# Performance work log

Measured on AMD Instinct MI355X. Metric: run time of the kernel, lower is better.

The kernel has to match this reference:

```python
import jax, jax.numpy as jnp
import numpy as np
import math

N_HEAD = 16
ROPE_BASE = 10000.0


def _rope_cos_sin(seq_len, head_dim, dtype):
    # standard RoPE tables: freqs_i = base^(-2i/d), i in [0, d/2)
    half = head_dim // 2
    inv_freq = ROPE_BASE ** (-(jnp.arange(half, dtype=jnp.float32) * 2.0 / head_dim))
    t = jnp.arange(seq_len, dtype=jnp.float32)
    ang = t[:, None] * inv_freq[None, :]  # [S, d/2]
    return jnp.cos(ang).astype(dtype), jnp.sin(ang).astype(dtype)


def _apply_rope(x, cos, sin):
    # x: [B, S, H, d]; rotate interleaved even/odd pairs
    x1 = x[..., 0::2]
    x2 = x[..., 1::2]
    c = cos[None, :, None, :]
    s = sin[None, :, None, :]
    out = jnp.stack([x1 * c - x2 * s, x1 * s + x2 * c], axis=-1)
    return out.reshape(x.shape)


def setup_inputs() -> dict:
    key = jax.random.key(0)
    kx, kq, kk, kv, ko = jax.random.split(key, 5)
    B, S, H = 2, 2048, 1024
    x = jax.random.normal(kx, (B, S, H), dtype=jnp.float32)
    scale = 0.02
    w_q = jax.random.normal(kq, (H, H), dtype=jnp.float32) * scale
    w_k = jax.random.normal(kk, (H, H), dtype=jnp.float32) * scale
    w_v = jax.random.normal(kv, (H, H), dtype=jnp.float32) * scale
    w_o = jax.random.normal(ko, (H, H), dtype=jnp.float32) * scale
    return {"x": x, "w_q": w_q, "w_k": w_k, "w_v": w_v, "w_o": w_o}


def reference(x, w_q, w_k, w_v, w_o):
    B, S, H = x.shape
    d = H // N_HEAD
    # torch nn.Linear(bias=False): y = x @ W^T, W is [out, in]
    q = (x @ w_q.T).reshape(B, S, N_HEAD, d)
    k = (x @ w_k.T).reshape(B, S, N_HEAD, d)
    v = (x @ w_v.T).reshape(B, S, N_HEAD, d)
    cos, sin = _rope_cos_sin(S, d, x.dtype)
    q = _apply_rope(q, cos, sin)
    k = _apply_rope(k, cos, sin)
    scores = jnp.einsum("bqhd,bkhd->bhqk", q, k) / math.sqrt(d)
    coefs = jax.nn.softmax(scores, axis=-1)
    # NOTE: causal mask is applied AFTER softmax via tril (no renormalization)
    causal = jnp.tril(jnp.ones((S, S), dtype=bool))
    coefs = jnp.where(causal[None, None], coefs, 0.0)
    out = jnp.einsum("bhqk,bkhd->bqhd", coefs, v).reshape(B, S, H)
    return out @ w_o.T
```

## Files before the change

### kernel.cpp

```cpp
#include <hip/hip_runtime.h>
#include <math.h>

#define SEQ   2048
#define HDIM  1024
#define NH    16
#define DH    64
#define MTOT  4096
#define BHTOT 32

typedef _Float16 half_t;
typedef __attribute__((ext_vector_type(2))) __fp16 fp16x2;
typedef __attribute__((ext_vector_type(4))) _Float16 half4;
typedef __attribute__((ext_vector_type(8))) _Float16 half8;
typedef __attribute__((ext_vector_type(4))) float float4v;

typedef __attribute__((address_space(1))) const unsigned int guint;
typedef __attribute__((address_space(3))) unsigned int luint;
__device__ __forceinline__ void glds16(const half_t* g, half_t* l) {
    __builtin_amdgcn_global_load_lds((guint*)g, (luint*)l, 16, 0, 0);
}

__global__ __launch_bounds__(256)
void prep(const float* __restrict__ x,  const float* __restrict__ wq,
          const float* __restrict__ wk, const float* __restrict__ wv,
          const float* __restrict__ wo,
          half_t* __restrict__ xh,  half_t* __restrict__ wqh,
          half_t* __restrict__ wkh, half_t* __restrict__ wvh,
          half_t* __restrict__ woh, float2* __restrict__ rope)
{
    const int bid = blockIdx.x;
    if (bid < 8192) {
        int i = bid * 256 + threadIdx.x;
        const float* s; half_t* d;
        if (i < 1048576) { s = x; d = xh; }
        else {
            int j = i - 1048576;
            int w = j >> 18; i = j & 262143;
            s = (w == 0) ? wq : (w == 1) ? wk : (w == 2) ? wv : wo;
            d = (w == 0) ? wqh : (w == 1) ? wkh : (w == 2) ? wvh : woh;
        }
        float4 v = ((const float4*)s)[i];
        union { half_t h[4]; uint2 u; } tmp;
        tmp.h[0] = (half_t)v.x; tmp.h[1] = (half_t)v.y;
        tmp.h[2] = (half_t)v.z; tmp.h[3] = (half_t)v.w;
        ((uint2*)d)[i] = tmp.u;
    } else {
        int tt = (bid - 8192) * 256 + threadIdx.x;
        int s = tt >> 5, j = tt & 31;
        float inv = powf(10000.0f, -(float)j / 32.0f);
        float ang = (float)s * inv;
        rope[tt] = make_float2(cosf(ang), sinf(ang));
    }
}

__global__ __launch_bounds__(256)
void gemm_qkv(const half_t* __restrict__ A,
              const half_t* __restrict__ w0, const half_t* __restrict__ w1,
              const half_t* __restrict__ w2,
              half_t* __restrict__ Qb, half_t* __restrict__ Kb,
              half_t* __restrict__ Vtb, float* __restrict__ outF,
              const float2* __restrict__ rope, int mode_base)
{
    const int mode = mode_base + blockIdx.z;
    const half_t* Bw = (mode == 1) ? w1 : (mode == 2) ? w2 : w0;

    __shared__ __align__(16) half_t Ash[128][32];
    __shared__ __align__(16) half_t Bsh[128][32];

    const int t    = threadIdx.x;
    const int lane = t & 63;
    const int wave = t >> 6;
    const int quad = lane >> 4;
    const int l16  = lane & 15;
    const int wr   = (wave >> 1) * 64;
    const int wc   = (wave & 1) * 64;
    const int bm   = blockIdx.x, bn = blockIdx.y;

    const int srow = lane >> 2, spos = lane & 3;
    const half_t* Asrc0 = A  + (size_t)(bm * 128 + wave * 32      + srow) * HDIM + spos * 8;
    const half_t* Asrc1 = A  + (size_t)(bm * 128 + wave * 32 + 16 + srow) * HDIM + spos * 8;
    const half_t* Bsrc0 = Bw + (size_t)(bn * 128 + wave * 32      + srow) * HDIM + spos * 8;
    const half_t* Bsrc1 = Bw + (size_t)(bn * 128 + wave * 32 + 16 + srow) * HDIM + spos * 8;
    half_t* Adst0 = &Ash[wave * 32][0];
    half_t* Adst1 = &Ash[wave * 32 + 16][0];
    half_t* Bdst0 = &Bsh[wave * 32][0];
    half_t* Bdst1 = &Bsh[wave * 32 + 16][0];

    float4v acc[4][4] = {};

    for (int kt = 0; kt < HDIM / 32; ++kt) {
        glds16(Asrc0, Adst0);
        glds16(Asrc1, Adst1);
        glds16(Bsrc0, Bdst0);
        glds16(Bsrc1, Bdst1);
        Asrc0 += 32; Asrc1 += 32; Bsrc0 += 32; Bsrc1 += 32;
        __syncthreads();
        half8 af[4], bf[4];
#pragma unroll
        for (int mb = 0; mb < 4; ++mb) af[mb] = *(const half8*)&Ash[wr + mb * 16 + l16][quad * 8];
#pragma unroll
        for (int nb = 0; nb < 4; ++nb) bf[nb] = *(const half8*)&Bsh[wc + nb * 16 + l16][quad * 8];
#pragma unroll
        for (int mb = 0; mb < 4; ++mb)
#pragma unroll
            for (int nb = 0; nb < 4; ++nb)
                acc[mb][nb] = __builtin_amdgcn_mfma_f32_16x16x32_f16(af[mb], bf[nb], acc[mb][nb], 0, 0, 0);
        __syncthreads();
    }

    if (mode == 3) {
#pragma unroll
        for (int mb = 0; mb < 4; ++mb)
#pragma unroll
            for (int nb = 0; nb < 4; ++nb) {
                int row0 = bm * 128 + wr + mb * 16 + quad * 4;
                int col  = bn * 128 + wc + nb * 16 + l16;
#pragma unroll
                for (int r = 0; r < 4; ++r)
                    outF[(size_t)(row0 + r) * HDIM + col] = acc[mb][nb][r];
            }
        return;
    }
    if (mode == 2) {
#pragma unroll
        for (int mb = 0; mb < 4; ++mb)
#pragma unroll
            for (int nb = 0; nb < 4; ++nb) {
                int row0 = bm * 128 + wr + mb * 16 + quad * 4;
                int col  = bn * 128 + wc + nb * 16 + l16;
                int b = row0 >> 11, s0 = row0 & 2047;
                int h = col >> 6,  dd = col & 63;
                union { half_t h4[4]; uint2 u; } tmp;
#pragma unroll
                for (int r = 0; r < 4; ++r) tmp.h4[r] = (half_t)acc[mb][nb][r];
                *(uint2*)&Vtb[((size_t)((b * NH + h) * DH + dd)) * SEQ + s0] = tmp.u;
            }
        return;
    }
    {
        half_t* Ob = (mode == 0) ? Qb : Kb;
        const float scl = (mode == 0) ? 0.125f * 1.44269504088896f : 1.0f;
#pragma unroll
        for (int mb = 0; mb < 4; ++mb)
#pragma unroll
            for (int nb = 0; nb < 4; ++nb) {
                int row0 = bm * 128 + wr + mb * 16 + quad * 4;
                int col  = bn * 128 + wc + nb * 16 + l16;
                int b = row0 >> 11;
                int h = col >> 6, dd = col & 63, j = dd >> 1;
#pragma unroll
                for (int r = 0; r < 4; ++r) {
                    float v  = acc[mb][nb][r];
                    float vp = __shfl_xor(v, 1, 64);
                    int s = (row0 + r) & 2047;
                    float2 cs = rope[s * 32 + j];
                    float res = ((col & 1) == 0) ? (v * cs.x - vp * cs.y)
                                                 : (vp * cs.y + v * cs.x);
                    Ob[((size_t)((b * NH + h) * SEQ + s)) * DH + dd] = (half_t)(res * scl);
                }
            }
    }
}

__global__ __launch_bounds__(256)
void attn_fused(const half_t* __restrict__ Qb, const half_t* __restrict__ Kb,
                const half_t* __restrict__ Vtb, half_t* __restrict__ AOut)
{
    const int qt = blockIdx.x;
    const int bh = blockIdx.y;

    __shared__ __align__(16) half_t Ksh[2][64][64];
    __shared__ __align__(16) half_t Vsh[2][64][72];

    const int t = threadIdx.x;
    const int wave = t >> 6, lane = t & 63, quad = lane >> 4, l16 = lane & 15;
    const int q0 = qt * 128 + wave * 32;

    half8 qf[2][2];
#pragma unroll
    for (int g = 0; g < 2; ++g) {
        const half_t* Qp = Qb + ((size_t)bh * SEQ + q0 + g * 16 + l16) * DH + quad * 8;
        qf[g][0] = *(const half8*)Qp;
        qf[g][1] = *(const half8*)(Qp + 32);
    }

    float4v o[2][4] = {};
    float lsum[2] = {0.f, 0.f};

    const int krow = lane >> 3, kpos = lane & 7;
    const int kchunk = kpos ^ krow;
    const half_t* Ksrc0 = Kb + ((size_t)bh * SEQ + wave * 16     + krow) * DH + kchunk * 8;
    const half_t* Ksrc1 = Kb + ((size_t)bh * SEQ + wave * 16 + 8 + krow) * DH + kchunk * 8;
    const int ko1 = ((quad ^ (l16 & 7)) * 8);
    const int ko2 = ko1 ^ 32;

    const int sr  = t >> 2;
    const int scc = (t & 3) * 16;
    const half_t* Vg = Vtb + ((size_t)bh * DH + sr) * SEQ + scc;

    glds16(Ksrc0, &Ksh[0][wave * 16][0]);
    glds16(Ksrc1, &Ksh[0][wave * 16 + 8][0]);
    *(uint4*)&Vsh[0][sr][scc]     = *(const uint4*)(Vg);
    *(uint4*)&Vsh[0][sr][scc + 8] = *(const uint4*)(Vg + 8);
    __syncthreads();

    const int qmax = qt * 128 + 127;
    for (int kt = 0; kt < SEQ / 64; ++kt) {
        const int cur = kt & 1, nxt = cur ^ 1;
        const bool have_next = (kt + 1 < SEQ / 64);
        const bool next_v    = ((kt + 1) * 64 <= qmax);

        uint4 va, vb;
        if (have_next) {
            const half_t* Kn = Ksrc0 + (size_t)(kt + 1) * 64 * DH;
            glds16(Kn,          &Ksh[nxt][wave * 16][0]);
            glds16(Kn + 8 * DH, &Ksh[nxt][wave * 16 + 8][0]);
            if (next_v) {
                const half_t* Vgk = Vg + (kt + 1) * 64;
                va = *(const uint4*)(Vgk);
                vb = *(const uint4*)(Vgk + 8);
            }
        }

        float4v sc[2][4];
#pragma unroll
        for (int nb = 0; nb < 4; ++nb) {
            const half_t* kp = &Ksh[cur][nb * 16 + l16][0];
            half8 kf0 = *(const half8*)(kp + ko1);
            half8 kf1 = *(const half8*)(kp + ko2);
#pragma unroll
            for (int g = 0; g < 2; ++g) {
                float4v a = {};
                a = __builtin_amdgcn_mfma_f32_16x16x32_f16(kf0, qf[g][0], a, 0, 0, 0);
                a = __builtin_amdgcn_mfma_f32_16x16x32_f16(kf1, qf[g][1], a, 0, 0, 0);
                sc[g][nb] = a;
            }
        }

#pragma unroll
        for (int g = 0; g < 2; ++g)
#pragma unroll
            for (int nb = 0; nb < 4; ++nb)
#pragma unroll
                for (int r = 0; r < 4; ++r) {
                    float e = __builtin_amdgcn_exp2f(sc[g][nb][r]);
                    sc[g][nb][r] = e;
                    lsum[g] += e;
                }

        const int kbase = kt * 64;
        if (kbase <= q0 + 31) {
            if (kbase + 63 > q0) {
#pragma unroll
                for (int g = 0; g < 2; ++g) {
                    int qg = q0 + g * 16 + l16;
#pragma unroll
                    for (int nb = 0; nb < 4; ++nb)
#pragma unroll
                        for (int r = 0; r < 4; ++r)
                            if (kbase + nb * 16 + quad * 4 + r > qg) sc[g][nb][r] = 0.f;
                }
            }
            half4 pf[2][4];
#pragma unroll
            for (int g = 0; g < 2; ++g)
#pragma unroll
                for (int nb = 0; nb < 4; ++nb) {
                    union { fp16x2 v2[2]; half4 v4; } u;
                    u.v2[0] = __builtin_amdgcn_cvt_pkrtz(sc[g][nb][0], sc[g][nb][1]);
                    u.v2[1] = __builtin_amdgcn_cvt_pkrtz(sc[g][nb][2], sc[g][nb][3]);
                    pf[g][nb] = u.v4;
                }
#pragma unroll
            for (int md = 0; md < 4; ++md)
#pragma unroll
                for (int nb = 0; nb < 4; ++nb) {
                    half4 vf = *(const half4*)&Vsh[cur][md * 16 + l16][nb * 16 + quad * 4];
                    o[0][md] = __builtin_amdgcn_mfma_f32_16x16x16f16(vf, pf[0][nb], o[0][md], 0, 0, 0);
                    o[1][md] = __builtin_amdgcn_mfma_f32_16x16x16f16(vf, pf[1][nb], o[1][md], 0, 0, 0);
                }
        }

        if (have_next && next_v) {
            *(uint4*)&Vsh[nxt][sr][scc]     = va;
            *(uint4*)&Vsh[nxt][sr][scc + 8] = vb;
        }
        __syncthreads();
    }

    const int b = bh >> 4, h = bh & 15;
    const int orow = lane >> 2, occ = (lane & 3) * 16;
#pragma unroll
    for (int g = 0; g < 2; ++g) {
        float rs = lsum[g];
        rs += __shfl_xor(rs, 16, 64);
        rs += __shfl_xor(rs, 32, 64);
        const float inv = 1.0f / rs;
        half_t (*Osh)[72] = (half_t(*)[72]) & Vsh[g][wave * 16][0];
#pragma unroll
        for (int md = 0; md < 4; ++md)
#pragma unroll
            for (int r = 0; r < 4; ++r)
                Osh[l16][md * 16 + quad * 4 + r] = (half_t)(o[g][md][r] * inv);
        __asm__ volatile("s_waitcnt lgkmcnt(0)" ::: "memory");
        uint4 o0 = *(const uint4*)&Osh[orow][occ];
        uint4 o1 = *(const uint4*)&Osh[orow][occ + 8];
        const int s = qt * 128 + wave * 32 + g * 16 + orow;
        half_t* dst = AOut + ((size_t)(b * SEQ + s)) * HDIM + h * DH + occ;
        *(uint4*)dst       = o0;
        *(uint4*)(dst + 8) = o1;
    }
}

extern "C" void kernel_launch(void* const* d_in, const int* in_sizes, int n_in,
                              void* d_out, int out_size, void* d_ws, size_t ws_size,
                              hipStream_t stream)
{
    const float* x  = (const float*)d_in[0];
    const float* wq = (const float*)d_in[1];
    const float* wk = (const float*)d_in[2];
    const float* wv = (const float*)d_in[3];
    const float* wo = (const float*)d_in[4];
    float* out = (float*)d_out;

    char* ws = (char*)d_ws;
    size_t off = 0;
    auto alloc = [&](size_t bytes) -> void* {
        void* p = ws + off;
        off += (bytes + 255) & ~(size_t)255;
        return p;
    };
    half_t* xh   = (half_t*)alloc((size_t)MTOT * HDIM * 2);
    half_t* wqh  = (half_t*)alloc((size_t)HDIM * HDIM * 2);
    half_t* wkh  = (half_t*)alloc((size_t)HDIM * HDIM * 2);
    half_t* wvh  = (half_t*)alloc((size_t)HDIM * HDIM * 2);
    half_t* woh  = (half_t*)alloc((size_t)HDIM * HDIM * 2);
    half_t* Qb   = (half_t*)alloc((size_t)BHTOT * SEQ * DH * 2);
    half_t* Kb   = (half_t*)alloc((size_t)BHTOT * SEQ * DH * 2);
    half_t* Vtb  = (half_t*)alloc((size_t)BHTOT * SEQ * DH * 2);
    half_t* ah   = (half_t*)alloc((size_t)MTOT * HDIM * 2);
    float2* rope = (float2*)alloc((size_t)SEQ * 32 * sizeof(float2));

    prep<<<8448, 256, 0, stream>>>(x, wq, wk, wv, wo, xh, wqh, wkh, wvh, woh, rope);

    gemm_qkv<<<dim3(32, 8, 3), 256, 0, stream>>>(xh, wqh, wkh, wvh,
                                                 Qb, Kb, Vtb, nullptr, rope, 0);
    attn_fused<<<dim3(16, 32), 256, 0, stream>>>(Qb, Kb, Vtb, ah);
    gemm_qkv<<<dim3(32, 8, 1), 256, 0, stream>>>(ah, woh, woh, woh,
                                                 nullptr, nullptr, nullptr, out, rope, 3);
}
```

Measured before the change: 207.2 us.

## Pair low and high query tiles per block to balance causal attention work

Each block now handles one 64-row query tile from the top of the sequence and its mirror tile from the bottom, instead of a contiguous 128-row tile. This evens out causal P·V work across blocks and waves, so the blocks with few active key tiles no longer leave the GPU waiting on the heaviest blocks. The P·V MFMAs for the low tile are skipped once it passes its causal limit. The QK/exp work still covers all key tiles, as before, because the row sums run over the full sequence. The launch grid presumably stays 16 tiles per head.

```diff
diff --git a/kernel.cpp b/kernel.cpp
--- a/kernel.cpp
+++ b/kernel.cpp
@@ -174,14 +174,18 @@
 
     const int t = threadIdx.x;
     const int wave = t >> 6, lane = t & 63, quad = lane >> 4, l16 = lane & 15;
-    const int q0 = qt * 128 + wave * 32;
+
+    const int qb0 = qt * 64 + wave * 16;
+    const int qb1 = (31 - qt) * 64 + wave * 16;
 
     half8 qf[2][2];
-#pragma unroll
-    for (int g = 0; g < 2; ++g) {
-        const half_t* Qp = Qb + ((size_t)bh * SEQ + q0 + g * 16 + l16) * DH + quad * 8;
-        qf[g][0] = *(const half8*)Qp;
-        qf[g][1] = *(const half8*)(Qp + 32);
+    {
+        const half_t* Qp0 = Qb + ((size_t)bh * SEQ + qb0 + l16) * DH + quad * 8;
+        qf[0][0] = *(const half8*)Qp0;
+        qf[0][1] = *(const half8*)(Qp0 + 32);
+        const half_t* Qp1 = Qb + ((size_t)bh * SEQ + qb1 + l16) * DH + quad * 8;
+        qf[1][0] = *(const half8*)Qp1;
+        qf[1][1] = *(const half8*)(Qp1 + 32);
     }
 
     float4v o[2][4] = {};
@@ -204,11 +208,11 @@
     *(uint4*)&Vsh[0][sr][scc + 8] = *(const uint4*)(Vg + 8);
     __syncthreads();
 
-    const int qmax = qt * 128 + 127;
+    const int ktop = 31 - qt;
     for (int kt = 0; kt < SEQ / 64; ++kt) {
         const int cur = kt & 1, nxt = cur ^ 1;
         const bool have_next = (kt + 1 < SEQ / 64);
-        const bool next_v    = ((kt + 1) * 64 <= qmax);
+        const bool next_v    = (kt + 1 <= ktop);
 
         uint4 va, vb;
         if (have_next) {
@@ -249,35 +253,48 @@
                 }
 
         const int kbase = kt * 64;
-        if (kbase <= q0 + 31) {
-            if (kbase + 63 > q0) {
-#pragma unroll
-                for (int g = 0; g < 2; ++g) {
-                    int qg = q0 + g * 16 + l16;
-#pragma unroll
-                    for (int nb = 0; nb < 4; ++nb)
-#pragma unroll
-                        for (int r = 0; r < 4; ++r)
-                            if (kbase + nb * 16 + quad * 4 + r > qg) sc[g][nb][r] = 0.f;
+        const bool act1 = (kbase <= qb1 + 15);
+        const bool act0 = (kbase <= qb0 + 15);
+        if (act1) {
+            if (kbase + 63 > qb1) {
+#pragma unroll
+                for (int nb = 0; nb < 4; ++nb)
+#pragma unroll
+                    for (int r = 0; r < 4; ++r)
+                        if (kbase + nb * 16 + quad * 4 + r > qb1 + l16) sc[1][nb][r] = 0.f;
+            }
+            if (act0 && (kbase + 63 > qb0)) {
+#pragma unroll
+                for (int nb = 0; nb < 4; ++nb)
+#pragma unroll
+                    for (int r = 0; r < 4; ++r)
+                        if (kbase + nb * 16 + quad * 4 + r > qb0 + l16) sc[0][nb][r] = 0.f;
+            }
+            half4 pf[2][4];
+#pragma unroll
+            for (int nb = 0; nb < 4; ++nb) {
+                union { fp16x2 v2[2]; half4 v4; } u1;
+                u1.v2[0] = __builtin_amdgcn_cvt_pkrtz(sc[1][nb][0], sc[1][nb][1]);
+                u1.v2[1] = __builtin_amdgcn_cvt_pkrtz(sc[1][nb][2], sc[1][nb][3]);
+                pf[1][nb] = u1.v4;
+            }
+            if (act0) {
+#pragma unroll
+                for (int nb = 0; nb < 4; ++nb) {
+                    union { fp16x2 v2[2]; half4 v4; } u0;
+                    u0.v2[0] = __builtin_amdgcn_cvt_pkrtz(sc[0][nb][0], sc[0][nb][1]);
+                    u0.v2[1] = __builtin_amdgcn_cvt_pkrtz(sc[0][nb][2], sc[0][nb][3]);
+                    pf[0][nb] = u0.v4;
                 }
             }
-            half4 pf[2][4];
-#pragma unroll
-            for (int g = 0; g < 2; ++g)
-#pragma unroll
-                for (int nb = 0; nb < 4; ++nb) {
-                    union { fp16x2 v2[2]; half4 v4; } u;
-                    u.v2[0] = __builtin_amdgcn_cvt_pkrtz(sc[g][nb][0], sc[g][nb][1]);
-                    u.v2[1] = __builtin_amdgcn_cvt_pkrtz(sc[g][nb][2], sc[g][nb][3]);
-                    pf[g][nb] = u.v4;
-                }
 #pragma unroll
             for (int md = 0; md < 4; ++md)
 #pragma unroll
                 for (int nb = 0; nb < 4; ++nb) {
                     half4 vf = *(const half4*)&Vsh[cur][md * 16 + l16][nb * 16 + quad * 4];
-                    o[0][md] = __builtin_amdgcn_mfma_f32_16x16x16f16(vf, pf[0][nb], o[0][md], 0, 0, 0);
                     o[1][md] = __builtin_amdgcn_mfma_f32_16x16x16f16(vf, pf[1][nb], o[1][md], 0, 0, 0);
+                    if (act0)
+                        o[0][md] = __builtin_amdgcn_mfma_f32_16x16x16f16(vf, pf[0][nb], o[0][md], 0, 0, 0);
                 }
         }
 
@@ -305,7 +322,7 @@
         __asm__ volatile("s_waitcnt lgkmcnt(0)" ::: "memory");
         uint4 o0 = *(const uint4*)&Osh[orow][occ];
         uint4 o1 = *(const uint4*)&Osh[orow][occ + 8];
-        const int s = qt * 128 + wave * 32 + g * 16 + orow;
+        const int s = ((g == 0) ? qt : (31 - qt)) * 64 + wave * 16 + orow;
         half_t* dst = AOut + ((size_t)(b * SEQ + s)) * HDIM + h * DH + occ;
         *(uint4*)dst       = o0;
         *(uint4*)(dst + 8) = o1;
```

New measurement: 212.7 us. 2.6% more time.

## Pair complementary causal query tiles per block and coalesce Q/K epilogue stores

Applied to the files above, without the earlier changes.

The attention kernel now runs 512 threads per block, pairing query tile jb with tile 15-jb. Both tiles share the K/V loads, and the work per block evens out because the causal PV cost grows with the tile index. K loads are issued by one half of the block and V loads by the other. The Q/K GEMM epilogue now stages rope-rotated results in shared memory and writes 16-byte coalesced rows instead of scattered 2-byte stores. This adds LDS use and larger blocks, which may reduce occupancy.

```diff
diff --git a/kernel.cpp b/kernel.cpp
--- a/kernel.cpp
+++ b/kernel.cpp
@@ -66,6 +66,7 @@
 
     __shared__ __align__(16) half_t Ash[128][32];
     __shared__ __align__(16) half_t Bsh[128][32];
+    __shared__ __align__(16) half_t Esh[4][32][72];
 
     const int t    = threadIdx.x;
     const int lane = t & 63;
@@ -140,33 +141,48 @@
     {
         half_t* Ob = (mode == 0) ? Qb : Kb;
         const float scl = (mode == 0) ? 0.125f * 1.44269504088896f : 1.0f;
-#pragma unroll
-        for (int mb = 0; mb < 4; ++mb)
-#pragma unroll
-            for (int nb = 0; nb < 4; ++nb) {
-                int row0 = bm * 128 + wr + mb * 16 + quad * 4;
-                int col  = bn * 128 + wc + nb * 16 + l16;
-                int b = row0 >> 11;
-                int h = col >> 6, dd = col & 63, j = dd >> 1;
-#pragma unroll
-                for (int r = 0; r < 4; ++r) {
-                    float v  = acc[mb][nb][r];
-                    float vp = __shfl_xor(v, 1, 64);
-                    int s = (row0 + r) & 2047;
-                    float2 cs = rope[s * 32 + j];
-                    float res = ((col & 1) == 0) ? (v * cs.x - vp * cs.y)
-                                                 : (vp * cs.y + v * cs.x);
-                    Ob[((size_t)((b * NH + h) * SEQ + s)) * DH + dd] = (half_t)(res * scl);
-                }
-            }
-    }
-}
-
-__global__ __launch_bounds__(256)
+        const int h = (bn * 128 + wc) >> 6;
+#pragma unroll
+        for (int mh = 0; mh < 2; ++mh) {
+#pragma unroll
+            for (int mb2 = 0; mb2 < 2; ++mb2) {
+                const int mb = mh * 2 + mb2;
+                const int row0 = bm * 128 + wr + mb * 16 + quad * 4;
+#pragma unroll
+                for (int nb = 0; nb < 4; ++nb) {
+                    const int dd = nb * 16 + l16;
+                    const int jj = dd >> 1;
+#pragma unroll
+                    for (int r = 0; r < 4; ++r) {
+                        float v  = acc[mb][nb][r];
+                        float vp = __shfl_xor(v, 1, 64);
+                        int s = (row0 + r) & 2047;
+                        float2 cs = rope[s * 32 + jj];
+                        float res = ((dd & 1) == 0) ? (v * cs.x - vp * cs.y)
+                                                    : (vp * cs.y + v * cs.x);
+                        Esh[wave][mb2 * 16 + quad * 4 + r][dd] = (half_t)(res * scl);
+                    }
+                }
+            }
+            __asm__ volatile("s_waitcnt lgkmcnt(0)" ::: "memory");
+#pragma unroll
+            for (int c = 0; c < 4; ++c) {
+                int uidx = c * 64 + lane;
+                int row = uidx >> 3, ch = uidx & 7;
+                uint4 v = *(const uint4*)&Esh[wave][row][ch * 8];
+                int sg = bm * 128 + wr + mh * 32 + row;
+                int b = sg >> 11, s = sg & 2047;
+                *(uint4*)&Ob[((size_t)((b * NH + h) * SEQ + s)) * DH + ch * 8] = v;
+            }
+        }
+    }
+}
+
+__global__ __launch_bounds__(512)
 void attn_fused(const half_t* __restrict__ Qb, const half_t* __restrict__ Kb,
                 const half_t* __restrict__ Vtb, half_t* __restrict__ AOut)
 {
-    const int qt = blockIdx.x;
+    const int jb = blockIdx.x;
     const int bh = blockIdx.y;
 
     __shared__ __align__(16) half_t Ksh[2][64][64];
@@ -174,7 +190,10 @@
 
     const int t = threadIdx.x;
     const int wave = t >> 6, lane = t & 63, quad = lane >> 4, l16 = lane & 15;
-    const int q0 = qt * 128 + wave * 32;
+    const int unit = wave >> 2, wl = wave & 3;
+    const int qtile = unit ? (15 - jb) : jb;
+    const int q0 = qtile * 128 + wl * 32;
+    const int ktop = 2 * (15 - jb) + 1;
 
     half8 qf[2][2];
 #pragma unroll
@@ -189,37 +208,41 @@
 
     const int krow = lane >> 3, kpos = lane & 7;
     const int kchunk = kpos ^ krow;
-    const half_t* Ksrc0 = Kb + ((size_t)bh * SEQ + wave * 16     + krow) * DH + kchunk * 8;
-    const half_t* Ksrc1 = Kb + ((size_t)bh * SEQ + wave * 16 + 8 + krow) * DH + kchunk * 8;
+    const half_t* Ksrc0 = Kb + ((size_t)bh * SEQ + wl * 16     + krow) * DH + kchunk * 8;
+    const half_t* Ksrc1 = Kb + ((size_t)bh * SEQ + wl * 16 + 8 + krow) * DH + kchunk * 8;
     const int ko1 = ((quad ^ (l16 & 7)) * 8);
     const int ko2 = ko1 ^ 32;
 
-    const int sr  = t >> 2;
-    const int scc = (t & 3) * 16;
+    const int tv  = t & 255;
+    const int sr  = tv >> 2;
+    const int scc = (tv & 3) * 16;
     const half_t* Vg = Vtb + ((size_t)bh * DH + sr) * SEQ + scc;
 
-    glds16(Ksrc0, &Ksh[0][wave * 16][0]);
-    glds16(Ksrc1, &Ksh[0][wave * 16 + 8][0]);
-    *(uint4*)&Vsh[0][sr][scc]     = *(const uint4*)(Vg);
-    *(uint4*)&Vsh[0][sr][scc + 8] = *(const uint4*)(Vg + 8);
+    if (unit == 0) {
+        glds16(Ksrc0, &Ksh[0][wl * 16][0]);
+        glds16(Ksrc1, &Ksh[0][wl * 16 + 8][0]);
+    } else {
+        *(uint4*)&Vsh[0][sr][scc]     = *(const uint4*)(Vg);
+        *(uint4*)&Vsh[0][sr][scc + 8] = *(const uint4*)(Vg + 8);
+    }
     __syncthreads();
 
-    const int qmax = qt * 128 + 127;
     for (int kt = 0; kt < SEQ / 64; ++kt) {
         const int cur = kt & 1, nxt = cur ^ 1;
         const bool have_next = (kt + 1 < SEQ / 64);
-        const bool next_v    = ((kt + 1) * 64 <= qmax);
+        const bool next_v    = (kt + 1 <= ktop);
 
         uint4 va, vb;
-        if (have_next) {
-            const half_t* Kn = Ksrc0 + (size_t)(kt + 1) * 64 * DH;
-            glds16(Kn,          &Ksh[nxt][wave * 16][0]);
-            glds16(Kn + 8 * DH, &Ksh[nxt][wave * 16 + 8][0]);
-            if (next_v) {
-                const half_t* Vgk = Vg + (kt + 1) * 64;
-                va = *(const uint4*)(Vgk);
-                vb = *(const uint4*)(Vgk + 8);
-            }
+        if (unit == 0) {
+            if (have_next) {
+                const half_t* Kn = Ksrc0 + (size_t)(kt + 1) * 64 * DH;
+                glds16(Kn,          &Ksh[nxt][wl * 16][0]);
+                glds16(Kn + 8 * DH, &Ksh[nxt][wl * 16 + 8][0]);
+            }
+        } else if (have_next && next_v) {
+            const half_t* Vgk = Vg + (kt + 1) * 64;
+            va = *(const uint4*)(Vgk);
+            vb = *(const uint4*)(Vgk + 8);
         }
 
         float4v sc[2][4];
@@ -281,7 +304,7 @@
                 }
         }
 
-        if (have_next && next_v) {
+        if (unit == 1 && have_next && next_v) {
             *(uint4*)&Vsh[nxt][sr][scc]     = va;
             *(uint4*)&Vsh[nxt][sr][scc + 8] = vb;
         }
@@ -290,13 +313,14 @@
 
     const int b = bh >> 4, h = bh & 15;
     const int orow = lane >> 2, occ = (lane & 3) * 16;
+    half_t* scr = unit ? ((half_t*)Vsh + wl * 1152) : ((half_t*)Ksh + wl * 1152);
+    half_t (*Osh)[72] = (half_t(*)[72])scr;
 #pragma unroll
     for (int g = 0; g < 2; ++g) {
         float rs = lsum[g];
         rs += __shfl_xor(rs, 16, 64);
         rs += __shfl_xor(rs, 32, 64);
         const float inv = 1.0f / rs;
-        half_t (*Osh)[72] = (half_t(*)[72]) & Vsh[g][wave * 16][0];
 #pragma unroll
         for (int md = 0; md < 4; ++md)
 #pragma unroll
@@ -305,7 +329,7 @@
         __asm__ volatile("s_waitcnt lgkmcnt(0)" ::: "memory");
         uint4 o0 = *(const uint4*)&Osh[orow][occ];
         uint4 o1 = *(const uint4*)&Osh[orow][occ + 8];
-        const int s = qt * 128 + wave * 32 + g * 16 + orow;
+        const int s = q0 + g * 16 + orow;
         half_t* dst = AOut + ((size_t)(b * SEQ + s)) * HDIM + h * DH + occ;
         *(uint4*)dst       = o0;
         *(uint4*)(dst + 8) = o1;
@@ -345,7 +369,7 @@
 
     gemm_qkv<<<dim3(32, 8, 3), 256, 0, stream>>>(xh, wqh, wkh, wvh,
                                                  Qb, Kb, Vtb, nullptr, rope, 0);
-    attn_fused<<<dim3(16, 32), 256, 0, stream>>>(Qb, Kb, Vtb, ah);
+    attn_fused<<<dim3(8, 32), 512, 0, stream>>>(Qb, Kb, Vtb, ah);
     gemm_qkv<<<dim3(32, 8, 1), 256, 0, stream>>>(ah, woh, woh, woh,
                                                  nullptr, nullptr, nullptr, out, rope, 3);
 }
```

Result: faster. 195.3 us (-5.7%).
